# Kernel optimization log

Measured on AMD Instinct MI355X. Metric: run time of the kernel, lower is better.

Reference implementation:

```python
import jax, jax.numpy as jnp
import numpy as np

N = 100000  # nodes
E = 1600000  # edges
F = 128      # nfeat == nclass (source constructs every layer as nfeat->nclass)


def setup_inputs() -> dict:
    key = jax.random.key(0)
    ks = jax.random.split(key, 8)
    x = jax.random.normal(ks[0], (N, F), dtype=jnp.float32)
    row = jax.random.randint(ks[1], (E,), 0, N)
    col = jax.random.randint(ks[2], (E,), 0, N)
    s = (1.0 / np.sqrt(F)).astype(np.float32) if hasattr(1.0/np.sqrt(F), 'astype') else 1.0/np.sqrt(F)
    s = 1.0 / np.sqrt(F)
    W0 = jax.random.uniform(ks[3], (F, F), jnp.float32, -s, s)
    b0 = jax.random.uniform(ks[4], (F,), jnp.float32, -s, s)
    W1 = jax.random.uniform(ks[5], (F, F), jnp.float32, -s, s)
    b1 = jax.random.uniform(ks[6], (F,), jnp.float32, -s, s)
    return {"x": x, "W0": W0, "b0": b0, "W1": W1, "b1": b1, "row": row, "col": col}


def _gcn_layer(h_in, W, b, row, col, dinv):
    # h = Linear(feat)
    h = h_in @ W + b
    # (D^-1/2 (A+I) D^-1/2) @ h, A in COO (row=i, col=j), A[i,j]=1
    coef = dinv[row] * dinv[col]                      # [E]
    msg = h[col] * coef[:, None]                       # [E, F] gather
    agg = jax.ops.segment_sum(msg, row, num_segments=N)
    agg = agg + (dinv * dinv)[:, None] * h             # self loops (identity)
    return agg


def reference(x, W0, b0, W1, b1, row, col):
    # D_hat = diag((A + I).sum(0)) -> column sums + 1
    deg = jax.ops.segment_sum(jnp.ones((E,), jnp.float32), col, num_segments=N) + 1.0
    dinv = deg ** -0.5
    h = _gcn_layer(x, W0, b0, row, col, dinv)
    h = jax.nn.relu(h)            # with_relu=True; dropout off (eval mode)
    h = _gcn_layer(h, W1, b1, row, col, dinv)
    return jax.nn.log_softmax(h, axis=1)
```

## Files before the change

kernel.cpp:

```cpp
#include <hip/hip_runtime.h>
#include <math.h>

#define FDIM 128
#define RPB 128
#define BSTRIDE 32
#define NBLK 256
#define MAXB 1024

typedef __attribute__((ext_vector_type(8))) short short8;
typedef __attribute__((ext_vector_type(4))) float floatx4;

static __device__ __forceinline__ unsigned short f2bf(float f) {
    unsigned int u = __float_as_uint(f);
    u = (u + 0x7fff + ((u >> 16) & 1)) >> 16;
    return (unsigned short)u;
}

static __device__ __forceinline__ unsigned int cvtpk(float a, float b) {
    unsigned int r;
    asm("v_cvt_pk_bf16_f32 %0, %1, %2" : "=v"(r) : "v"(a), "v"(b));
    return r;
}

static __device__ __forceinline__ void bf2f(unsigned int u, float& a, float& b) {
    a = __uint_as_float(u << 16);
    b = __uint_as_float(u & 0xffff0000u);
}


__global__ __launch_bounds__(256) void k_zero(int* rbCnt, int* cbCnt, int nbs, unsigned int* hsz) {
    int i = blockIdx.x * 256 + threadIdx.x;
    if (i < nbs) { rbCnt[i] = 0; cbCnt[i] = 0; }
    if (blockIdx.x == 0 && threadIdx.x < 64) hsz[threadIdx.x] = 0u;
}

__global__ __launch_bounds__(256) void k_count(const int* __restrict__ row, const int* __restrict__ col,
                                               int* rbCnt, int* cbCnt, int nE, int nb) {
    __shared__ int rh[MAXB];
    __shared__ int ch[MAXB];
    const int tid = threadIdx.x;
    const int cpb = (nE + NBLK - 1) / NBLK;
    const int e0 = blockIdx.x * cpb;
    int e1 = e0 + cpb; if (e1 > nE) e1 = nE;
    for (int i = tid; i < nb; i += 256) { rh[i] = 0; ch[i] = 0; }
    __syncthreads();
    for (int e = e0 + tid; e < e1; e += 256) {
        atomicAdd(&rh[row[e] >> 7], 1);
        atomicAdd(&ch[col[e] >> 7], 1);
    }
    __syncthreads();
    for (int i = tid; i < nb; i += 256) {
        if (rh[i]) atomicAdd(&rbCnt[(size_t)i * BSTRIDE], rh[i]);
        if (ch[i]) atomicAdd(&cbCnt[(size_t)i * BSTRIDE], ch[i]);
    }
}

__global__ __launch_bounds__(1024) void k_bscan(const int* __restrict__ rbCnt, const int* __restrict__ cbCnt,
                                                int* rbBase, int* cbBase, int* rbCur, int* cbCur,
                                                int nb, int nE) {
    __shared__ int s[1024];
    int tid = threadIdx.x;
    int v = (tid < nb) ? rbCnt[(size_t)tid * BSTRIDE] : 0;
    s[tid] = v;
    __syncthreads();
    for (int off = 1; off < 1024; off <<= 1) {
        int t = (tid >= off) ? s[tid - off] : 0;
        __syncthreads();
        s[tid] += t;
        __syncthreads();
    }
    if (tid < nb) {
        int ex = s[tid] - v;
        rbBase[tid] = ex;
        rbCur[(size_t)tid * BSTRIDE] = ex;
    }
    if (tid == 0) rbBase[nb] = nE;
    __syncthreads();
    v = (tid < nb) ? cbCnt[(size_t)tid * BSTRIDE] : 0;
    s[tid] = v;
    __syncthreads();
    for (int off = 1; off < 1024; off <<= 1) {
        int t = (tid >= off) ? s[tid - off] : 0;
        __syncthreads();
        s[tid] += t;
        __syncthreads();
    }
    if (tid < nb) {
        int ex = s[tid] - v;
        cbBase[tid] = ex;
        cbCur[(size_t)tid * BSTRIDE] = ex;
    }
    if (tid == 0) cbBase[nb] = nE;
}

__global__ __launch_bounds__(256) void k_scatter2(const int* __restrict__ row, const int* __restrict__ col,
                                                  int* rbCur, int* cbCur,
                                                  unsigned int* __restrict__ pairs,
                                                  unsigned char* __restrict__ clocal, int nE, int nb) {
    __shared__ int rh[MAXB];
    __shared__ int ch[MAXB];
    __shared__ int rbase[MAXB];
    __shared__ int cbase[MAXB];
    const int tid = threadIdx.x;
    const int cpb = (nE + NBLK - 1) / NBLK;
    const int e0 = blockIdx.x * cpb;
    int e1 = e0 + cpb; if (e1 > nE) e1 = nE;

    for (int i = tid; i < nb; i += 256) { rh[i] = 0; ch[i] = 0; }
    __syncthreads();
    for (int e = e0 + tid; e < e1; e += 256) {
        atomicAdd(&rh[row[e] >> 7], 1);
        atomicAdd(&ch[col[e] >> 7], 1);
    }
    __syncthreads();
    for (int i = tid; i < nb; i += 256) {
        rbase[i] = rh[i] ? atomicAdd(&rbCur[(size_t)i * BSTRIDE], rh[i]) : 0;
        cbase[i] = ch[i] ? atomicAdd(&cbCur[(size_t)i * BSTRIDE], ch[i]) : 0;
        rh[i] = 0;
        ch[i] = 0;
    }
    __syncthreads();
    for (int e = e0 + tid; e < e1; e += 256) {
        int r = row[e];
        int c = col[e];
        int rb = r >> 7, cb = c >> 7;
        int p = rbase[rb] + atomicAdd(&rh[rb], 1);
        pairs[p] = ((unsigned int)(r & (RPB - 1)) << 25) | (unsigned int)c;
        int q = cbase[cb] + atomicAdd(&ch[cb], 1);
        clocal[q] = (unsigned char)(c & (RPB - 1));
    }
}

__global__ __launch_bounds__(256) void k_rowsort(const int* __restrict__ rbBase,
                                                 const unsigned int* __restrict__ pairs,
                                                 int* __restrict__ row_ptr, int* __restrict__ csr_col,
                                                 int n, int nb) {
    __shared__ int hist[RPB];
    __shared__ int scan[RPB];
    __shared__ int lcur[RPB];
    const int b = blockIdx.x;
    const int tid = threadIdx.x;
    const int row0 = b * RPB;
    const int start = rbBase[b];
    const int endp = rbBase[b + 1];

    if (tid < RPB) hist[tid] = 0;
    __syncthreads();
    for (int i = start + tid; i < endp; i += 256)
        atomicAdd(&hist[pairs[i] >> 25], 1);
    __syncthreads();

    if (tid < RPB) scan[tid] = hist[tid];
    __syncthreads();
    for (int off = 1; off < RPB; off <<= 1) {
        int t = (tid < RPB && tid >= off) ? scan[tid - off] : 0;
        __syncthreads();
        if (tid < RPB) scan[tid] += t;
        __syncthreads();
    }
    if (tid < RPB) {
        int ex = start + scan[tid] - hist[tid];
        lcur[tid] = ex;
        int r = row0 + tid;
        if (r < n) row_ptr[r] = ex;
    }
    if (b == nb - 1 && tid == 0) row_ptr[n] = endp;
    __syncthreads();

    for (int i = start + tid; i < endp; i += 256) {
        unsigned int u = pairs[i];
        int pos = atomicAdd(&lcur[u >> 25], 1);
        csr_col[pos] = (int)(u & 0x1FFFFFFu);
    }
}

__global__ __launch_bounds__(256) void k_colhist(const int* __restrict__ cbBase,
                                                 const unsigned char* __restrict__ clocal,
                                                 float* __restrict__ dinv, int n) {
    __shared__ int hist[RPB];
    const int b = blockIdx.x;
    const int tid = threadIdx.x;
    const int start = cbBase[b];
    const int endp = cbBase[b + 1];
    if (tid < RPB) hist[tid] = 0;
    __syncthreads();
    for (int i = start + tid; i < endp; i += 256)
        atomicAdd(&hist[(int)clocal[i]], 1);
    __syncthreads();
    if (tid < RPB) {
        int c = b * RPB + tid;
        if (c < n) dinv[c] = rsqrtf((float)hist[tid] + 1.0f);
    }
}


__global__ __launch_bounds__(256) void k_cvtW(const float* __restrict__ W0, const float* __restrict__ W1,
                                              unsigned short* __restrict__ W0t, unsigned short* __restrict__ W1t) {
    const float* W = blockIdx.x ? W1 : W0;
    unsigned short* Wt = blockIdx.x ? W1t : W0t;
    for (int idx = threadIdx.x; idx < FDIM * FDIM; idx += 256) {
        int k = idx >> 7, c = idx & 127;
        Wt[c * FDIM + k] = f2bf(W[idx]);
    }
}


#define KH 64
#define LPAD 72

__global__ __launch_bounds__(256) void k_gemm_mfma(const void* __restrict__ Ain,
                                                   const unsigned short* __restrict__ Wt,
                                                   const float* __restrict__ bias,
                                                   const float* __restrict__ dinv,
                                                   unsigned int* __restrict__ outp, int n, int af32) {
    __shared__ unsigned short sA[128][LPAD];
    __shared__ unsigned short sW[128][LPAD];

    const unsigned short* A = (const unsigned short*)Ain;
    const float* Af = (const float*)Ain;

    const int tid = threadIdx.x;
    const int row0 = blockIdx.x * 128;
    const int wid = tid >> 6;
    const int lane = tid & 63;
    const int quad = lane >> 4;
    const int lq = lane & 15;
    const int wm = wid & 1;
    const int wn = wid >> 1;

    floatx4 acc[4][4];
#pragma unroll
    for (int i = 0; i < 4; i++)
#pragma unroll
        for (int j = 0; j < 4; j++) acc[i][j] = (floatx4){0.f, 0.f, 0.f, 0.f};

    for (int kh = 0; kh < 2; kh++) {
        if (kh) __syncthreads();
#pragma unroll
        for (int it = 0; it < 4; it++) {
            int f = tid + it * 256;
            int r = f >> 3;
            int c8 = (f & 7) * 8;
            int gr = row0 + r;
            if (af32) {
                float4 v0 = make_float4(0.f, 0.f, 0.f, 0.f);
                float4 v1 = make_float4(0.f, 0.f, 0.f, 0.f);
                if (gr < n) {
                    v0 = *(const float4*)&Af[(size_t)gr * FDIM + kh * KH + c8];
                    v1 = *(const float4*)&Af[(size_t)gr * FDIM + kh * KH + c8 + 4];
                }
                uint4 p;
                p.x = cvtpk(v0.x, v0.y);
                p.y = cvtpk(v0.z, v0.w);
                p.z = cvtpk(v1.x, v1.y);
                p.w = cvtpk(v1.z, v1.w);
                *(uint4*)&sA[r][c8] = p;
            } else {
                uint4 v = make_uint4(0u, 0u, 0u, 0u);
                if (gr < n) v = *(const uint4*)&A[(size_t)gr * FDIM + kh * KH + c8];
                *(uint4*)&sA[r][c8] = v;
            }
            uint4 wv = *(const uint4*)&Wt[(size_t)r * FDIM + kh * KH + c8];
            *(uint4*)&sW[r][c8] = wv;
        }
        __syncthreads();

#pragma unroll
        for (int kt = 0; kt < 2; kt++) {
            const int k0 = kt * 32 + quad * 8;
            short8 af[4], bf[4];
#pragma unroll
            for (int mt = 0; mt < 4; mt++)
                af[mt] = *(const short8*)&sA[wm * 64 + mt * 16 + lq][k0];
#pragma unroll
            for (int nt = 0; nt < 4; nt++)
                bf[nt] = *(const short8*)&sW[wn * 64 + nt * 16 + lq][k0];
#pragma unroll
            for (int mt = 0; mt < 4; mt++)
#pragma unroll
                for (int nt = 0; nt < 4; nt++)
                    acc[mt][nt] = __builtin_amdgcn_mfma_f32_16x16x32_bf16(af[mt], bf[nt], acc[mt][nt], 0, 0, 0);
        }
    }

    float bv[4];
#pragma unroll
    for (int nt = 0; nt < 4; nt++) bv[nt] = bias[wn * 64 + nt * 16 + lq];

#pragma unroll
    for (int mt = 0; mt < 4; mt++) {
#pragma unroll
        for (int r = 0; r < 4; r++) {
            int grow = row0 + wm * 64 + mt * 16 + quad * 4 + r;
            float di = (grow < n) ? dinv[grow] : 0.f;
#pragma unroll
            for (int nt = 0; nt < 4; nt++) {
                float v = (acc[mt][nt][r] + bv[nt]) * di;
                float pv = __shfl_xor(v, 1, 64);
                if (!(lq & 1) && grow < n) {
                    int col = wn * 64 + nt * 16 + lq;
                    outp[(size_t)grow * 64 + (col >> 1)] =
                        (unsigned int)f2bf(v) | ((unsigned int)f2bf(pv) << 16);
                }
            }
        }
    }
}


#define GATH(i) int j##i = __builtin_amdgcn_readlane(jv, t + i); \
                unsigned int u##i = hs[(size_t)j##i * 64 + lane];

__global__ __launch_bounds__(256) void k_agg(const unsigned int* __restrict__ hs, const int* __restrict__ row_ptr,
                                             const int* __restrict__ csr_col, const float* __restrict__ dinv,
                                             void* __restrict__ out, int n, int relu, int lsm, int obf) {
    int w = (blockIdx.x * 256 + threadIdx.x) >> 6;
    int lane = threadIdx.x & 63;
    if (w >= n) return;
    float a0, a1;
    bf2f(hs[(size_t)w * 64 + lane], a0, a1);

    int e = row_ptr[w];
    const int end = row_ptr[w + 1];
    const int zrow = n;

    while (e < end) {
        int cnt = end - e;
        if (cnt > 64) cnt = 64;
        int jv = (e + lane < end) ? csr_col[e + lane] : zrow;
        for (int t = 0; t < cnt; t += 16) {
            GATH(0)  GATH(1)  GATH(2)  GATH(3)
            GATH(4)  GATH(5)  GATH(6)  GATH(7)
            GATH(8)  GATH(9)  GATH(10) GATH(11)
            GATH(12) GATH(13) GATH(14) GATH(15)
            float x0, y0, x1, y1, x2, y2, x3, y3, x4, y4, x5, y5, x6, y6, x7, y7;
            float x8, y8, x9, y9, x10, y10, x11, y11, x12, y12, x13, y13, x14, y14, x15, y15;
            bf2f(u0, x0, y0);   bf2f(u1, x1, y1);   bf2f(u2, x2, y2);   bf2f(u3, x3, y3);
            bf2f(u4, x4, y4);   bf2f(u5, x5, y5);   bf2f(u6, x6, y6);   bf2f(u7, x7, y7);
            bf2f(u8, x8, y8);   bf2f(u9, x9, y9);   bf2f(u10, x10, y10); bf2f(u11, x11, y11);
            bf2f(u12, x12, y12); bf2f(u13, x13, y13); bf2f(u14, x14, y14); bf2f(u15, x15, y15);
            a0 += ((((x0 + x1) + (x2 + x3)) + ((x4 + x5) + (x6 + x7))) +
                   (((x8 + x9) + (x10 + x11)) + ((x12 + x13) + (x14 + x15))));
            a1 += ((((y0 + y1) + (y2 + y3)) + ((y4 + y5) + (y6 + y7))) +
                   (((y8 + y9) + (y10 + y11)) + ((y12 + y13) + (y14 + y15))));
        }
        e += cnt;
    }

    float di = dinv[w];
    a0 *= di;
    a1 *= di;
    if (relu) {
        a0 = fmaxf(a0, 0.0f);
        a1 = fmaxf(a1, 0.0f);
    }
    if (lsm) {
        float m = fmaxf(a0, a1);
#pragma unroll
        for (int off = 32; off > 0; off >>= 1) m = fmaxf(m, __shfl_xor(m, off, 64));
        float s = expf(a0 - m) + expf(a1 - m);
#pragma unroll
        for (int off = 32; off > 0; off >>= 1) s += __shfl_xor(s, off, 64);
        float lg = m + logf(s);
        a0 -= lg;
        a1 -= lg;
    }
    if (obf) {
        ((unsigned int*)out)[(size_t)w * 64 + lane] =
            (unsigned int)f2bf(a0) | ((unsigned int)f2bf(a1) << 16);
    } else {
        ((float2*)out)[(size_t)w * 64 + lane] = make_float2(a0, a1);
    }
}


extern "C" void kernel_launch(void* const* d_in, const int* in_sizes, int n_in,
                              void* d_out, int out_size, void* d_ws, size_t ws_size,
                              hipStream_t stream) {
    const float* x  = (const float*)d_in[0];
    const float* W0 = (const float*)d_in[1];
    const float* b0 = (const float*)d_in[2];
    const float* W1 = (const float*)d_in[3];
    const float* b1 = (const float*)d_in[4];
    const int* row  = (const int*)d_in[5];
    const int* col  = (const int*)d_in[6];
    float* out = (float*)d_out;

    const int N = in_sizes[0] / FDIM;
    const int E = in_sizes[5];
    const int NB = (N + RPB - 1) / RPB;

    char* w = (char*)d_ws;
    size_t off = 0;
    auto alloc = [&](size_t bytes) {
        char* p = w + off;
        off += (bytes + 255) & ~(size_t)255;
        return p;
    };
    int* rbCnt   = (int*)alloc((size_t)NB * BSTRIDE * 4);
    int* cbCnt   = (int*)alloc((size_t)NB * BSTRIDE * 4);
    int* rbCur   = (int*)alloc((size_t)NB * BSTRIDE * 4);
    int* cbCur   = (int*)alloc((size_t)NB * BSTRIDE * 4);
    int* rbBase  = (int*)alloc((size_t)(NB + 1) * 4);
    int* cbBase  = (int*)alloc((size_t)(NB + 1) * 4);
    float* dinv  = (float*)alloc((size_t)N * 4);
    int* row_ptr = (int*)alloc((size_t)(N + 1) * 4);
    int* csr_col = (int*)alloc((size_t)E * 4);
    unsigned short* W0t = (unsigned short*)alloc((size_t)FDIM * FDIM * 2);
    unsigned short* W1t = (unsigned short*)alloc((size_t)FDIM * FDIM * 2);
    unsigned int* hs = (unsigned int*)alloc((size_t)(N + 1) * 64 * 4);
    size_t uniSz = (size_t)E * 4 + (size_t)E + 512;
    size_t hbSz  = (size_t)N * 64 * 4;
    char* uni = (char*)alloc(uniSz > hbSz ? uniSz : hbSz);
    unsigned int* pairs = (unsigned int*)uni;
    unsigned char* clocal = (unsigned char*)uni + (size_t)E * 4;
    unsigned int* hb = (unsigned int*)uni;

    const int gW = (N * 64 + 255) / 256;
    const int gG = (N + 127) / 128;
    const int gZ = (NB * BSTRIDE + 255) / 256;

    k_zero<<<gZ, 256, 0, stream>>>(rbCnt, cbCnt, NB * BSTRIDE, hs + (size_t)N * 64);
    k_count<<<NBLK, 256, 0, stream>>>(row, col, rbCnt, cbCnt, E, NB);
    k_bscan<<<1, 1024, 0, stream>>>(rbCnt, cbCnt, rbBase, cbBase, rbCur, cbCur, NB, E);
    k_scatter2<<<NBLK, 256, 0, stream>>>(row, col, rbCur, cbCur, pairs, clocal, E, NB);
    k_rowsort<<<NB, 256, 0, stream>>>(rbBase, pairs, row_ptr, csr_col, N, NB);
    k_colhist<<<NB, 256, 0, stream>>>(cbBase, clocal, dinv, N);

    k_cvtW<<<2, 256, 0, stream>>>(W0, W1, W0t, W1t);

    k_gemm_mfma<<<gG, 256, 0, stream>>>((const void*)x, W0t, b0, dinv, hs, N, 1);
    k_agg<<<gW, 256, 0, stream>>>(hs, row_ptr, csr_col, dinv, hb, N, 1, 0, 1);

    k_gemm_mfma<<<gG, 256, 0, stream>>>((const void*)hb, W1t, b1, dinv, hs, N, 0);
    k_agg<<<gW, 256, 0, stream>>>(hs, row_ptr, csr_col, dinv, out, N, 0, 1, 0);
}
```

Baseline: 397.5 us.

## Gather four neighbor rows per load with 16-byte vector reads split across wave quarters

Restructures the aggregation kernel so each quarter-wave of 16 lanes loads one neighbor row using 16-byte uint4 reads, handling four neighbors per load instruction instead of one 4-byte read per lane per neighbor. Partial sums from the four quarters are combined with cross-lane shuffles at the end, and the log-softmax and output stores are adapted to the 8-values-per-lane layout. This reduces the number of memory instructions and per-edge index broadcasts, at the cost of more accumulator registers and an extra shuffle reduction.

After: 392.3 us. About the same (-1.3%).

```diff
diff --git a/kernel.cpp b/kernel.cpp
--- a/kernel.cpp
+++ b/kernel.cpp
@@ -308,8 +308,11 @@
 }
 
 
-#define GATH(i) int j##i = __builtin_amdgcn_readlane(jv, t + i); \
-                unsigned int u##i = hs[(size_t)j##i * 64 + lane];
+#define UACC(U) { float p_, q_; \
+    bf2f(U.x, p_, q_); acc0 += p_; acc1 += q_; \
+    bf2f(U.y, p_, q_); acc2 += p_; acc3 += q_; \
+    bf2f(U.z, p_, q_); acc4 += p_; acc5 += q_; \
+    bf2f(U.w, p_, q_); acc6 += p_; acc7 += q_; }
 
 __global__ __launch_bounds__(256) void k_agg(const unsigned int* __restrict__ hs, const int* __restrict__ row_ptr,
                                              const int* __restrict__ csr_col, const float* __restrict__ dinv,
@@ -317,8 +320,16 @@
     int w = (blockIdx.x * 256 + threadIdx.x) >> 6;
     int lane = threadIdx.x & 63;
     if (w >= n) return;
-    float a0, a1;
-    bf2f(hs[(size_t)w * 64 + lane], a0, a1);
+    const int quad = lane >> 4;
+    const int lq = lane & 15;
+
+    uint4 sv = make_uint4(0u, 0u, 0u, 0u);
+    if (quad == 0) sv = *(const uint4*)&hs[(size_t)w * 64 + lq * 4];
+    float acc0, acc1, acc2, acc3, acc4, acc5, acc6, acc7;
+    bf2f(sv.x, acc0, acc1);
+    bf2f(sv.y, acc2, acc3);
+    bf2f(sv.z, acc4, acc5);
+    bf2f(sv.w, acc6, acc7);
 
     int e = row_ptr[w];
     const int end = row_ptr[w + 1];
@@ -328,48 +339,71 @@
         int cnt = end - e;
         if (cnt > 64) cnt = 64;
         int jv = (e + lane < end) ? csr_col[e + lane] : zrow;
-        for (int t = 0; t < cnt; t += 16) {
-            GATH(0)  GATH(1)  GATH(2)  GATH(3)
-            GATH(4)  GATH(5)  GATH(6)  GATH(7)
-            GATH(8)  GATH(9)  GATH(10) GATH(11)
-            GATH(12) GATH(13) GATH(14) GATH(15)
-            float x0, y0, x1, y1, x2, y2, x3, y3, x4, y4, x5, y5, x6, y6, x7, y7;
-            float x8, y8, x9, y9, x10, y10, x11, y11, x12, y12, x13, y13, x14, y14, x15, y15;
-            bf2f(u0, x0, y0);   bf2f(u1, x1, y1);   bf2f(u2, x2, y2);   bf2f(u3, x3, y3);
-            bf2f(u4, x4, y4);   bf2f(u5, x5, y5);   bf2f(u6, x6, y6);   bf2f(u7, x7, y7);
-            bf2f(u8, x8, y8);   bf2f(u9, x9, y9);   bf2f(u10, x10, y10); bf2f(u11, x11, y11);
-            bf2f(u12, x12, y12); bf2f(u13, x13, y13); bf2f(u14, x14, y14); bf2f(u15, x15, y15);
-            a0 += ((((x0 + x1) + (x2 + x3)) + ((x4 + x5) + (x6 + x7))) +
-                   (((x8 + x9) + (x10 + x11)) + ((x12 + x13) + (x14 + x15))));
-            a1 += ((((y0 + y1) + (y2 + y3)) + ((y4 + y5) + (y6 + y7))) +
-                   (((y8 + y9) + (y10 + y11)) + ((y12 + y13) + (y14 + y15))));
+        int nb16 = (cnt + 15) >> 4;
+        for (int t = 0; t < nb16; t++) {
+            int idx = t * 16 + quad;
+            int j0 = __shfl(jv, idx,      64);
+            int j1 = __shfl(jv, idx + 4,  64);
+            int j2 = __shfl(jv, idx + 8,  64);
+            int j3 = __shfl(jv, idx + 12, 64);
+            uint4 u0 = *(const uint4*)&hs[(size_t)j0 * 64 + lq * 4];
+            uint4 u1 = *(const uint4*)&hs[(size_t)j1 * 64 + lq * 4];
+            uint4 u2 = *(const uint4*)&hs[(size_t)j2 * 64 + lq * 4];
+            uint4 u3 = *(const uint4*)&hs[(size_t)j3 * 64 + lq * 4];
+            UACC(u0)
+            UACC(u1)
+            UACC(u2)
+            UACC(u3)
         }
         e += cnt;
     }
 
+    acc0 += __shfl_xor(acc0, 16, 64); acc0 += __shfl_xor(acc0, 32, 64);
+    acc1 += __shfl_xor(acc1, 16, 64); acc1 += __shfl_xor(acc1, 32, 64);
+    acc2 += __shfl_xor(acc2, 16, 64); acc2 += __shfl_xor(acc2, 32, 64);
+    acc3 += __shfl_xor(acc3, 16, 64); acc3 += __shfl_xor(acc3, 32, 64);
+    acc4 += __shfl_xor(acc4, 16, 64); acc4 += __shfl_xor(acc4, 32, 64);
+    acc5 += __shfl_xor(acc5, 16, 64); acc5 += __shfl_xor(acc5, 32, 64);
+    acc6 += __shfl_xor(acc6, 16, 64); acc6 += __shfl_xor(acc6, 32, 64);
+    acc7 += __shfl_xor(acc7, 16, 64); acc7 += __shfl_xor(acc7, 32, 64);
+
     float di = dinv[w];
-    a0 *= di;
-    a1 *= di;
+    acc0 *= di; acc1 *= di; acc2 *= di; acc3 *= di;
+    acc4 *= di; acc5 *= di; acc6 *= di; acc7 *= di;
     if (relu) {
-        a0 = fmaxf(a0, 0.0f);
-        a1 = fmaxf(a1, 0.0f);
+        acc0 = fmaxf(acc0, 0.f); acc1 = fmaxf(acc1, 0.f);
+        acc2 = fmaxf(acc2, 0.f); acc3 = fmaxf(acc3, 0.f);
+        acc4 = fmaxf(acc4, 0.f); acc5 = fmaxf(acc5, 0.f);
+        acc6 = fmaxf(acc6, 0.f); acc7 = fmaxf(acc7, 0.f);
     }
     if (lsm) {
-        float m = fmaxf(a0, a1);
-#pragma unroll
-        for (int off = 32; off > 0; off >>= 1) m = fmaxf(m, __shfl_xor(m, off, 64));
-        float s = expf(a0 - m) + expf(a1 - m);
-#pragma unroll
-        for (int off = 32; off > 0; off >>= 1) s += __shfl_xor(s, off, 64);
+        float m = fmaxf(fmaxf(fmaxf(acc0, acc1), fmaxf(acc2, acc3)),
+                        fmaxf(fmaxf(acc4, acc5), fmaxf(acc6, acc7)));
+#pragma unroll
+        for (int off = 1; off < 16; off <<= 1) m = fmaxf(m, __shfl_xor(m, off, 64));
+        float s = ((expf(acc0 - m) + expf(acc1 - m)) + (expf(acc2 - m) + expf(acc3 - m))) +
+                  ((expf(acc4 - m) + expf(acc5 - m)) + (expf(acc6 - m) + expf(acc7 - m)));
+#pragma unroll
+        for (int off = 1; off < 16; off <<= 1) s += __shfl_xor(s, off, 64);
         float lg = m + logf(s);
-        a0 -= lg;
-        a1 -= lg;
+        acc0 -= lg; acc1 -= lg; acc2 -= lg; acc3 -= lg;
+        acc4 -= lg; acc5 -= lg; acc6 -= lg; acc7 -= lg;
     }
     if (obf) {
-        ((unsigned int*)out)[(size_t)w * 64 + lane] =
-            (unsigned int)f2bf(a0) | ((unsigned int)f2bf(a1) << 16);
+        if (quad == 0) {
+            uint4 o;
+            o.x = (unsigned int)f2bf(acc0) | ((unsigned int)f2bf(acc1) << 16);
+            o.y = (unsigned int)f2bf(acc2) | ((unsigned int)f2bf(acc3) << 16);
+            o.z = (unsigned int)f2bf(acc4) | ((unsigned int)f2bf(acc5) << 16);
+            o.w = (unsigned int)f2bf(acc6) | ((unsigned int)f2bf(acc7) << 16);
+            *(uint4*)((unsigned int*)out + (size_t)w * 64 + lq * 4) = o;
+        }
     } else {
-        ((float2*)out)[(size_t)w * 64 + lane] = make_float2(a0, a1);
+        if (quad < 2) {
+            float4 o = quad ? make_float4(acc4, acc5, acc6, acc7)
+                            : make_float4(acc0, acc1, acc2, acc3);
+            *(float4*)((float*)out + (size_t)w * 128 + lq * 8 + quad * 4) = o;
+        }
     }
 }
 
```
